# Performance work log

Measured on AMD Instinct MI355X. Metric: run time of the kernel, lower is better.

The kernel has to match this reference:

```python
import jax, jax.numpy as jnp
import numpy as np

B, C, N = 64, 512, 512  # batch, channels (=in_dim), last dim (=in_dim)
OUT = 512
GROUPS = 32
EPS = 1e-5


def setup_inputs() -> dict:
    key = jax.random.key(0)
    ks = jax.random.split(key, 7)
    s = 1.0 / np.sqrt(C)
    return {
        "x": jax.random.normal(ks[0], (B, C, N), dtype=jnp.float32),
        "q_w": jax.random.normal(ks[1], (OUT, C), dtype=jnp.float32) * s,
        "q_b": jax.random.normal(ks[2], (OUT,), dtype=jnp.float32) * s,
        "k_w": jax.random.normal(ks[3], (OUT, C), dtype=jnp.float32) * s,
        "k_b": jax.random.normal(ks[4], (OUT,), dtype=jnp.float32) * s,
        "v_w": jax.random.normal(ks[5], (OUT, C), dtype=jnp.float32) * s,
        "v_b": jax.random.normal(ks[6], (OUT,), dtype=jnp.float32) * s,
        "gn_w": jnp.ones((C,), dtype=jnp.float32),
        "gn_b": jnp.zeros((C,), dtype=jnp.float32),
    }


def group_norm(x, w, b):
    # x: (B, C, N); 32 groups over channel dim, affine per-channel.
    Bb, Cc, Nn = x.shape
    xg = x.reshape(Bb, GROUPS, -1)
    mean = jnp.mean(xg, axis=-1, keepdims=True)
    var = jnp.var(xg, axis=-1, keepdims=True)
    xn = ((xg - mean) * jax.lax.rsqrt(var + EPS)).reshape(Bb, Cc, Nn)
    return xn * w[None, :, None] + b[None, :, None]


def reference(x, q_w, q_b, k_w, k_b, v_w, v_b, gn_w, gn_b):
    xn = group_norm(x, gn_w, gn_b)  # (B, C, N)
    # nn.Linear applies to the last dim (N == in_dim)
    q = jnp.einsum("bcn,dn->bcd", xn, q_w) + q_b  # (B, C, OUT)
    k = jnp.einsum("bcn,dn->bcd", xn, k_w) + k_b
    v = jnp.einsum("bcn,dn->bcd", xn, v_w) + v_b
    scale = 1.0 / jnp.sqrt(jnp.float32(OUT))
    scores = jnp.einsum("bqd,bkd->bqk", q, k) * scale  # (B, C, C)
    attn = jax.nn.softmax(scores, axis=-1)
    return jnp.einsum("bqk,bkd->bqd", attn, v)  # (B, C, OUT)
```

## Files before the change

### kernel.cpp

```cpp
#include <hip/hip_runtime.h>
#include <cstdint>

#define EPSV 1e-5f
#define SM_SCALE 0.044194173824159216f

typedef unsigned short u16;
typedef __attribute__((ext_vector_type(8))) short short8;
typedef __attribute__((ext_vector_type(4))) float f32x4;

__device__ __forceinline__ u16 f2bf(float f) {
  union { float f; uint32_t u; } v; v.f = f;
  return (u16)((v.u + 0x7FFFu + ((v.u >> 16) & 1u)) >> 16);
}

__device__ __forceinline__ void gload_lds16(const void* g, void* l) {
  __builtin_amdgcn_global_load_lds((const __attribute__((address_space(1))) void*)g,
                                   (__attribute__((address_space(3))) void*)l, 16, 0, 0);
}

__device__ __forceinline__ f32x4 mfma16(short8 a, short8 b, f32x4 c) {
  return __builtin_amdgcn_mfma_f32_16x16x32_bf16(a, b, c, 0, 0, 0);
}

__device__ __forceinline__ const short8* lds_frag(const u16* t, int row, int cc) {
  return reinterpret_cast<const short8*>(t + (size_t)(((row << 2) + (cc ^ ((row >> 1) & 3))) << 3));
}

#define WAIT_ENTER(N, is_tail)                                      \
  if (is_tail) { asm volatile("s_waitcnt vmcnt(0)" ::: "memory"); } \
  else         { asm volatile("s_waitcnt vmcnt(" #N ")" ::: "memory"); } \
  __builtin_amdgcn_s_barrier();                                     \
  asm volatile("" ::: "memory");

#define WAIT_EXIT()                                                 \
  asm volatile("s_waitcnt lgkmcnt(0)" ::: "memory");                \
  __builtin_amdgcn_s_barrier();                                     \
  asm volatile("" ::: "memory");

__global__ __launch_bounds__(256) void gn_fused_k(const float* __restrict__ x,
                                                  const float* __restrict__ gw,
                                                  const float* __restrict__ gb,
                                                  u16* __restrict__ xn) {
  __shared__ float xs[8192];
  __shared__ float ls[4], lss[4];
  const int bg = blockIdx.x;
  const int g = bg & 31;
  const float* p = x + (size_t)bg * 8192;
  float s = 0.f, ss = 0.f;
#pragma unroll
  for (int i = 0; i < 8; ++i) {
    const int idx = i * 1024 + threadIdx.x * 4;
    float4 v = *reinterpret_cast<const float4*>(p + idx);
    *reinterpret_cast<float4*>(xs + idx) = v;
    s += v.x + v.y + v.z + v.w;
    ss += v.x * v.x + v.y * v.y + v.z * v.z + v.w * v.w;
  }
  for (int off = 32; off; off >>= 1) { s += __shfl_xor(s, off); ss += __shfl_xor(ss, off); }
  const int w = threadIdx.x >> 6;
  if ((threadIdx.x & 63) == 0) { ls[w] = s; lss[w] = ss; }
  __syncthreads();
  s = ls[0] + ls[1] + ls[2] + ls[3];
  ss = lss[0] + lss[1] + lss[2] + lss[3];
  const float inv_n = 1.0f / 8192.f;
  const float mean = s * inv_n;
  const float rstd = rsqrtf(ss * inv_n - mean * mean + EPSV);
#pragma unroll
  for (int j = 0; j < 4; ++j) {
    const int idx = j * 2048 + threadIdx.x * 8;
    const int c = g * 16 + (idx >> 9);
    const float sc = gw[c] * rstd;
    const float sh = gb[c] - mean * sc;
    u16 o[8];
#pragma unroll
    for (int e = 0; e < 8; ++e) o[e] = f2bf(xs[idx + e] * sc + sh);
    *reinterpret_cast<uint4*>(xn + (size_t)bg * 8192 + idx) = *reinterpret_cast<const uint4*>(o);
  }
}

__global__ __launch_bounds__(256) void cast3_k(const float* __restrict__ a,
                                               const float* __restrict__ b2,
                                               const float* __restrict__ c,
                                               u16* __restrict__ oa, u16* __restrict__ ob,
                                               u16* __restrict__ oc) {
  const int which = blockIdx.x >> 7;
  const float* in = which == 0 ? a : (which == 1 ? b2 : c);
  u16* out = which == 0 ? oa : (which == 1 ? ob : oc);
  size_t base = (((size_t)(blockIdx.x & 127)) * 256 + threadIdx.x) * 8;
  float4 v0 = *reinterpret_cast<const float4*>(in + base);
  float4 v1 = *reinterpret_cast<const float4*>(in + base + 4);
  u16 o[8];
  o[0] = f2bf(v0.x); o[1] = f2bf(v0.y); o[2] = f2bf(v0.z); o[3] = f2bf(v0.w);
  o[4] = f2bf(v1.x); o[5] = f2bf(v1.y); o[6] = f2bf(v1.z); o[7] = f2bf(v1.w);
  *reinterpret_cast<uint4*>(out + base) = *reinterpret_cast<const uint4*>(o);
}

template <int OUT_MODE>
__global__ __launch_bounds__(512, 1) void gemm256_k(const u16* __restrict__ A, size_t sA,
                                                    const u16* __restrict__ Bm, size_t sB,
                                                    const float* __restrict__ bias,
                                                    void* __restrict__ out, size_t sO) {
  __shared__ u16 smem[65536];
  const int d = blockIdx.x;
  const int wgid = (d & 7) * 32 + (d >> 3);
  const int b = wgid >> 2;
  const int tile = wgid & 3;
  const int tm = (tile >> 1) * 256, tn = (tile & 1) * 256;
  const u16* Ab = A + (size_t)b * sA;
  const u16* Bb = Bm + (size_t)b * sB;
  const int tid = threadIdx.x, w = tid >> 6, lane = tid & 63;
  const int rh = w >> 2, cw = w & 3;
  const int frow = lane & 15, cc = lane >> 4;
  f32x4 acc[8][4] = {};
  short8 af[8], bfr[2];

#define STAGEH(Lofs, Gp)                                                       \
  {                                                                            \
    const u16* gsrc_ = (Gp);                                                   \
    _Pragma("unroll")                                                          \
    for (int p_ = 0; p_ < 2; ++p_) {                                           \
      const int row_ = p_ * 64 + (tid >> 3);                                   \
      const int slot_ = (tid & 7) ^ (row_ & 7);                                \
      gload_lds16(gsrc_ + (size_t)row_ * 512 + slot_ * 8,                      \
                  &smem[(Lofs) + p_ * 4096 + tid * 8]);                        \
    }                                                                          \
  }

#define PHASE(VMN, QB, KS, CP, ...)                                            \
  {                                                                            \
    asm volatile("s_waitcnt vmcnt(" #VMN ")" ::: "memory");                    \
    __builtin_amdgcn_s_barrier();                                              \
    asm volatile("" ::: "memory");                                             \
    _Pragma("unroll")                                                          \
    for (int j_ = 0; j_ < 2; ++j_) {                                           \
      const int lrb_ = (cw & 1) * 64 + (CP) * 32 + j_ * 16 + frow;             \
      bfr[j_] = *reinterpret_cast<const short8*>(                              \
          &smem[(QB) + 16384 + (cw >> 1) * 8192 + lrb_ * 64 +                  \
                (((KS) * 4 + cc) ^ (lrb_ & 7)) * 8]);                          \
    }                                                                          \
    if ((CP) == 0) {                                                           \
      _Pragma("unroll")                                                        \
      for (int ri_ = 0; ri_ < 8; ++ri_) {                                      \
        const int lra_ = ri_ * 16 + frow;                                      \
        af[ri_] = *reinterpret_cast<const short8*>(                            \
            &smem[(QB) + rh * 8192 + lra_ * 64 +                               \
                  (((KS) * 4 + cc) ^ (lra_ & 7)) * 8]);                        \
      }                                                                        \
    }                                                                          \
    __VA_ARGS__                                                                \
    __builtin_amdgcn_s_setprio(1);                                             \
    _Pragma("unroll")                                                          \
    for (int ri_ = 0; ri_ < 8; ++ri_) {                                        \
      acc[ri_][(CP) * 2]     = mfma16(af[ri_], bfr[0], acc[ri_][(CP) * 2]);    \
      acc[ri_][(CP) * 2 + 1] = mfma16(af[ri_], bfr[1], acc[ri_][(CP) * 2 + 1]);\
    }                                                                          \
    __builtin_amdgcn_s_setprio(0);                                             \
    __builtin_amdgcn_s_barrier();                                              \
    asm volatile("" ::: "memory");                                             \
  }

  STAGEH(0,     Ab + (size_t)tm * 512);
  STAGEH(8192,  Ab + (size_t)(tm + 128) * 512);
  STAGEH(16384, Bb + (size_t)tn * 512);
  STAGEH(24576, Bb + (size_t)(tn + 128) * 512);
  STAGEH(32768, Ab + (size_t)tm * 512 + 64);

  for (int i = 0; i < 3; ++i) {
    const int k0c1 = i * 128 + 64;
    const int k0n2 = i * 128 + 128;
    const int k0n3 = i * 128 + 192;
    PHASE(2, 0, 0, 0,
          STAGEH(40960, Ab + (size_t)(tm + 128) * 512 + k0c1);
          STAGEH(49152, Bb + (size_t)tn * 512 + k0c1);)
    PHASE(6, 0, 0, 1,
          STAGEH(57344, Bb + (size_t)(tn + 128) * 512 + k0c1);)
    PHASE(6, 0, 1, 0, )
    PHASE(2, 0, 1, 1,
          STAGEH(0, Ab + (size_t)tm * 512 + k0n2);)
    PHASE(2, 32768, 0, 0,
          STAGEH(8192,  Ab + (size_t)(tm + 128) * 512 + k0n2);
          STAGEH(16384, Bb + (size_t)tn * 512 + k0n2);)
    PHASE(6, 32768, 0, 1,
          STAGEH(24576, Bb + (size_t)(tn + 128) * 512 + k0n2);)
    PHASE(6, 32768, 1, 0, )
    PHASE(2, 32768, 1, 1,
          STAGEH(32768, Ab + (size_t)tm * 512 + k0n3);)
  }
  PHASE(2, 0, 0, 0,
        STAGEH(40960, Ab + (size_t)(tm + 128) * 512 + 448);
        STAGEH(49152, Bb + (size_t)tn * 512 + 448);)
  PHASE(6, 0, 0, 1,
        STAGEH(57344, Bb + (size_t)(tn + 128) * 512 + 448);)
  PHASE(6, 0, 1, 0, )
  PHASE(2, 0, 1, 1, )
  PHASE(0, 32768, 0, 0, )
  PHASE(0, 32768, 0, 1, )
  PHASE(0, 32768, 1, 0, )
  PHASE(0, 32768, 1, 1, )
#undef PHASE
#undef STAGEH

  const int col0 = lane & 15, row0 = (lane >> 4) * 4;
#pragma unroll
  for (int ri = 0; ri < 8; ++ri) {
#pragma unroll
    for (int cj = 0; cj < 4; ++cj) {
      const int gc = tn + cw * 64 + cj * 16 + col0;
      const float bv = (OUT_MODE == 0) ? bias[gc] : 0.f;
#pragma unroll
      for (int r = 0; r < 4; ++r) {
        const int gr = tm + rh * 128 + ri * 16 + row0 + r;
        float v = acc[ri][cj][r];
        if (OUT_MODE == 0) v += bv;
        if (OUT_MODE == 1) v += bias[gr];
        if (OUT_MODE == 2)
          ((float*)out)[(size_t)b * sO + (size_t)gr * 512 + gc] = v;
        else
          ((u16*)out)[(size_t)b * sO + (size_t)gr * 512 + gc] = f2bf(v);
      }
    }
  }
}

__global__ __launch_bounds__(256, 2) void scores_softmax_k(const u16* __restrict__ Q,
                                                           const u16* __restrict__ K,
                                                           u16* __restrict__ P) {
  __shared__ u16 Qs[2][2048];
  __shared__ u16 Ks[2][16384];
  __shared__ float rmax[4][64], rsum[4][64];
  const int d = blockIdx.x;
  const int t = d >> 3;
  const int b = (d & 7) * 8 + (t >> 3);
  const int m0 = (t & 7) * 64;
  const u16* Qb = Q + (size_t)b * 262144 + (size_t)m0 * 512;
  const u16* Kb = K + (size_t)b * 262144;
  u16* Pb = P + (size_t)b * 262144;
  const int tid = threadIdx.x, kq = tid >> 6, lane = tid & 63;
  const int srow = lane >> 2;
  const int ssw = ((lane & 3) ^ ((lane >> 3) & 3)) * 8;
  f32x4 acc[4][8] = {};

#define SC_STAGE(bb, k0)                                                       \
  {                                                                            \
    _Pragma("unroll")                                                          \
    for (int s2 = 0; s2 < 8; ++s2) {                                           \
      const int c = kq * 8 + s2;                                               \
      gload_lds16(Kb + (size_t)(c * 16 + srow) * 512 + (k0) + ssw,             \
                  &Ks[bb][c * 512]);                                           \
    }                                                                          \
    gload_lds16(Qb + (size_t)(kq * 16 + srow) * 512 + (k0) + ssw,              \
                &Qs[bb][kq * 512]);                                            \
  }

  SC_STAGE(0, 0);
  SC_STAGE(1, 32);
  for (int ts = 0; ts < 16; ++ts) {
    const int cur = ts & 1;
    WAIT_ENTER(9, ts == 15);
    const int frow = lane & 15, cc = lane >> 4;
    short8 aq[4];
#pragma unroll
    for (int i = 0; i < 4; ++i)
      aq[i] = *lds_frag(Qs[cur], i * 16 + frow, cc);
#pragma unroll
    for (int j = 0; j < 8; ++j) {
      short8 bk = *lds_frag(Ks[cur], kq * 128 + j * 16 + frow, cc);
#pragma unroll
      for (int i = 0; i < 4; ++i)
        acc[i][j] = mfma16(aq[i], bk, acc[i][j]);
    }
    WAIT_EXIT();
    if (ts < 14) SC_STAGE(cur, (ts + 2) * 32);
  }
#undef SC_STAGE

  float pm[4][4];
#pragma unroll
  for (int i = 0; i < 4; ++i)
#pragma unroll
    for (int r = 0; r < 4; ++r) pm[i][r] = -1e30f;
#pragma unroll
  for (int i = 0; i < 4; ++i)
#pragma unroll
    for (int j = 0; j < 8; ++j)
#pragma unroll
      for (int r = 0; r < 4; ++r) {
        float v = acc[i][j][r] * SM_SCALE;
        acc[i][j][r] = v;
        pm[i][r] = fmaxf(pm[i][r], v);
      }
#pragma unroll
  for (int off = 1; off < 16; off <<= 1)
#pragma unroll
    for (int i = 0; i < 4; ++i)
#pragma unroll
      for (int r = 0; r < 4; ++r) pm[i][r] = fmaxf(pm[i][r], __shfl_xor(pm[i][r], off));
  if ((lane & 15) == 0) {
#pragma unroll
    for (int i = 0; i < 4; ++i)
#pragma unroll
      for (int r = 0; r < 4; ++r)
        rmax[kq][i * 16 + (lane >> 4) * 4 + r] = pm[i][r];
  }
  __syncthreads();
#pragma unroll
  for (int i = 0; i < 4; ++i)
#pragma unroll
    for (int r = 0; r < 4; ++r) {
      const int row = i * 16 + (lane >> 4) * 4 + r;
      pm[i][r] = fmaxf(fmaxf(rmax[0][row], rmax[1][row]), fmaxf(rmax[2][row], rmax[3][row]));
    }
  float ps[4][4];
#pragma unroll
  for (int i = 0; i < 4; ++i)
#pragma unroll
    for (int r = 0; r < 4; ++r) ps[i][r] = 0.f;
#pragma unroll
  for (int i = 0; i < 4; ++i)
#pragma unroll
    for (int j = 0; j < 8; ++j)
#pragma unroll
      for (int r = 0; r < 4; ++r) {
        float e = __expf(acc[i][j][r] - pm[i][r]);
        acc[i][j][r] = e;
        ps[i][r] += e;
      }
#pragma unroll
  for (int off = 1; off < 16; off <<= 1)
#pragma unroll
    for (int i = 0; i < 4; ++i)
#pragma unroll
      for (int r = 0; r < 4; ++r) ps[i][r] += __shfl_xor(ps[i][r], off);
  if ((lane & 15) == 0) {
#pragma unroll
    for (int i = 0; i < 4; ++i)
#pragma unroll
      for (int r = 0; r < 4; ++r)
        rsum[kq][i * 16 + (lane >> 4) * 4 + r] = ps[i][r];
  }
  __syncthreads();
#pragma unroll
  for (int i = 0; i < 4; ++i)
#pragma unroll
    for (int r = 0; r < 4; ++r) {
      const int row = i * 16 + (lane >> 4) * 4 + r;
      ps[i][r] = 1.0f / (rsum[0][row] + rsum[1][row] + rsum[2][row] + rsum[3][row]);
    }
#pragma unroll
  for (int i = 0; i < 4; ++i)
#pragma unroll
    for (int j = 0; j < 8; ++j) {
      const int gcol = kq * 128 + j * 16 + (lane & 15);
#pragma unroll
      for (int r = 0; r < 4; ++r) {
        const int grow = m0 + i * 16 + (lane >> 4) * 4 + r;
        Pb[(size_t)grow * 512 + gcol] = f2bf(acc[i][j][r] * ps[i][r]);
      }
    }
}

extern "C" void kernel_launch(void* const* d_in, const int* in_sizes, int n_in,
                              void* d_out, int out_size, void* d_ws, size_t ws_size,
                              hipStream_t stream) {
  const float* x = (const float*)d_in[0];
  const float* qw = (const float*)d_in[1];
  const float* qb = (const float*)d_in[2];
  const float* kw = (const float*)d_in[3];
  const float* kb = (const float*)d_in[4];
  const float* vw = (const float*)d_in[5];
  const float* vb = (const float*)d_in[6];
  const float* gnw = (const float*)d_in[7];
  const float* gnb = (const float*)d_in[8];

  char* ws = (char*)d_ws;
  u16* qwb = (u16*)(ws);
  u16* kwb = (u16*)(ws + 524288);
  u16* vwb = (u16*)(ws + 2 * 524288);
  u16* xn = (u16*)(ws + 4 * 524288);
  u16* Qb = xn + 16777216;
  u16* Kb = Qb + 16777216;
  u16* VT = Kb + 16777216;
  u16* P = xn;
  float* out = (float*)d_out;

  gn_fused_k<<<dim3(2048), dim3(256), 0, stream>>>(x, gnw, gnb, xn);
  cast3_k<<<dim3(384), dim3(256), 0, stream>>>(qw, kw, vw, qwb, kwb, vwb);
  gemm256_k<0><<<dim3(256), dim3(512), 0, stream>>>(xn, (size_t)262144, qwb, (size_t)0, qb, (void*)Qb, (size_t)262144);
  gemm256_k<0><<<dim3(256), dim3(512), 0, stream>>>(xn, (size_t)262144, kwb, (size_t)0, kb, (void*)Kb, (size_t)262144);
  gemm256_k<1><<<dim3(256), dim3(512), 0, stream>>>(vwb, (size_t)0, xn, (size_t)262144, vb, (void*)VT, (size_t)262144);
  scores_softmax_k<<<dim3(512), dim3(256), 0, stream>>>(Qb, Kb, P);
  gemm256_k<2><<<dim3(256), dim3(512), 0, stream>>>(P, (size_t)262144, VT, (size_t)262144, (const float*)nullptr, (void*)out, (size_t)262144);
}
```

Before: 148.1 us.

## Retile scores-softmax kernel to 128-row blocks with 8 waves and triple buffering

Rewrites the fused QK^T plus softmax kernel so each 512-thread workgroup handles 128 query rows instead of 64, with 8 waves each owning 64 key columns. This halves how often each K tile is reloaded per batch. The K/Q staging moves to a three-slot ring, with the next load issued after fragments are read so that only one barrier is needed per k-step. MFMA sections run at raised wave priority. The costs are a larger accumulator (32 fragments per wave), more LDS, one workgroup per CU and 256 blocks, which reduces occupancy and latency hiding.

```diff
diff --git a/kernel.cpp b/kernel.cpp
--- a/kernel.cpp
+++ b/kernel.cpp
@@ -21,21 +21,6 @@
 __device__ __forceinline__ f32x4 mfma16(short8 a, short8 b, f32x4 c) {
   return __builtin_amdgcn_mfma_f32_16x16x32_bf16(a, b, c, 0, 0, 0);
 }
-
-__device__ __forceinline__ const short8* lds_frag(const u16* t, int row, int cc) {
-  return reinterpret_cast<const short8*>(t + (size_t)(((row << 2) + (cc ^ ((row >> 1) & 3))) << 3));
-}
-
-#define WAIT_ENTER(N, is_tail)                                      \
-  if (is_tail) { asm volatile("s_waitcnt vmcnt(0)" ::: "memory"); } \
-  else         { asm volatile("s_waitcnt vmcnt(" #N ")" ::: "memory"); } \
-  __builtin_amdgcn_s_barrier();                                     \
-  asm volatile("" ::: "memory");
-
-#define WAIT_EXIT()                                                 \
-  asm volatile("s_waitcnt lgkmcnt(0)" ::: "memory");                \
-  __builtin_amdgcn_s_barrier();                                     \
-  asm volatile("" ::: "memory");
 
 __global__ __launch_bounds__(256) void gn_fused_k(const float* __restrict__ x,
                                                   const float* __restrict__ gw,
@@ -221,139 +206,156 @@
   }
 }
 
-__global__ __launch_bounds__(256, 2) void scores_softmax_k(const u16* __restrict__ Q,
+__global__ __launch_bounds__(512, 1) void scores_softmax_k(const u16* __restrict__ Q,
                                                            const u16* __restrict__ K,
                                                            u16* __restrict__ P) {
-  __shared__ u16 Qs[2][2048];
-  __shared__ u16 Ks[2][16384];
-  __shared__ float rmax[4][64], rsum[4][64];
+  __shared__ u16 smem[61440];
+  __shared__ float rmax[128][8], rsum[128][8];
   const int d = blockIdx.x;
-  const int t = d >> 3;
-  const int b = (d & 7) * 8 + (t >> 3);
-  const int m0 = (t & 7) * 64;
+  const int wgid = (d & 7) * 32 + (d >> 3);
+  const int b = wgid >> 2;
+  const int m0 = (wgid & 3) * 128;
   const u16* Qb = Q + (size_t)b * 262144 + (size_t)m0 * 512;
   const u16* Kb = K + (size_t)b * 262144;
-  u16* Pb = P + (size_t)b * 262144;
-  const int tid = threadIdx.x, kq = tid >> 6, lane = tid & 63;
-  const int srow = lane >> 2;
-  const int ssw = ((lane & 3) ^ ((lane >> 3) & 3)) * 8;
-  f32x4 acc[4][8] = {};
-
-#define SC_STAGE(bb, k0)                                                       \
+  u16* Pb = P + (size_t)b * 262144 + (size_t)m0 * 512;
+  const int tid = threadIdx.x, w = tid >> 6, lane = tid & 63;
+  const int frow = lane & 15, cc = lane >> 4;
+  f32x4 acc[8][4] = {};
+
+#define KQ_STAGE(m, k0)                                                        \
   {                                                                            \
     _Pragma("unroll")                                                          \
-    for (int s2 = 0; s2 < 8; ++s2) {                                           \
-      const int c = kq * 8 + s2;                                               \
-      gload_lds16(Kb + (size_t)(c * 16 + srow) * 512 + (k0) + ssw,             \
-                  &Ks[bb][c * 512]);                                           \
-    }                                                                          \
-    gload_lds16(Qb + (size_t)(kq * 16 + srow) * 512 + (k0) + ssw,              \
-                &Qs[bb][kq * 512]);                                            \
-  }
-
-  SC_STAGE(0, 0);
-  SC_STAGE(1, 32);
+    for (int s2_ = 0; s2_ < 4; ++s2_) {                                        \
+      const int idx_ = s2_ * 512 + tid;                                        \
+      const int row_ = idx_ >> 2, slot_ = idx_ & 3;                            \
+      gload_lds16(Kb + (size_t)row_ * 512 + (k0) + (slot_ ^ ((row_ >> 1) & 3)) * 8, \
+                  &smem[(m) * 16384 + idx_ * 8]);                              \
+    }                                                                          \
+    {                                                                          \
+      const int row_ = tid >> 2, slot_ = tid & 3;                              \
+      gload_lds16(Qb + (size_t)row_ * 512 + (k0) + (slot_ ^ ((row_ >> 1) & 3)) * 8, \
+                  &smem[49152 + (m) * 4096 + tid * 8]);                        \
+    }                                                                          \
+  }
+
+  KQ_STAGE(0, 0);
+  KQ_STAGE(1, 32);
   for (int ts = 0; ts < 16; ++ts) {
-    const int cur = ts & 1;
-    WAIT_ENTER(9, ts == 15);
-    const int frow = lane & 15, cc = lane >> 4;
-    short8 aq[4];
-#pragma unroll
-    for (int i = 0; i < 4; ++i)
-      aq[i] = *lds_frag(Qs[cur], i * 16 + frow, cc);
-#pragma unroll
-    for (int j = 0; j < 8; ++j) {
-      short8 bk = *lds_frag(Ks[cur], kq * 128 + j * 16 + frow, cc);
-#pragma unroll
-      for (int i = 0; i < 4; ++i)
-        acc[i][j] = mfma16(aq[i], bk, acc[i][j]);
-    }
-    WAIT_EXIT();
-    if (ts < 14) SC_STAGE(cur, (ts + 2) * 32);
-  }
-#undef SC_STAGE
-
-  float pm[4][4];
-#pragma unroll
-  for (int i = 0; i < 4; ++i)
-#pragma unroll
-    for (int r = 0; r < 4; ++r) pm[i][r] = -1e30f;
-#pragma unroll
-  for (int i = 0; i < 4; ++i)
-#pragma unroll
-    for (int j = 0; j < 8; ++j)
+    const int m = ts % 3;
+    if (ts < 15) { asm volatile("s_waitcnt vmcnt(5)" ::: "memory"); }
+    else         { asm volatile("s_waitcnt vmcnt(0)" ::: "memory"); }
+    __builtin_amdgcn_s_barrier();
+    asm volatile("" ::: "memory");
+    const u16* Kbuf = &smem[m * 16384];
+    const u16* Qbuf = &smem[49152 + m * 4096];
+    short8 af[8], bf[4];
+#pragma unroll
+    for (int ri = 0; ri < 8; ++ri) {
+      const int qrow = ri * 16 + frow;
+      af[ri] = *reinterpret_cast<const short8*>(
+          &Qbuf[qrow * 32 + ((cc ^ ((qrow >> 1) & 3)) * 8)]);
+    }
+#pragma unroll
+    for (int cj = 0; cj < 4; ++cj) {
+      const int krow = w * 64 + cj * 16 + frow;
+      bf[cj] = *reinterpret_cast<const short8*>(
+          &Kbuf[krow * 32 + ((cc ^ ((krow >> 1) & 3)) * 8)]);
+    }
+    if (ts < 14) KQ_STAGE((ts + 2) % 3, (ts + 2) * 32);
+    __builtin_amdgcn_s_setprio(1);
+#pragma unroll
+    for (int ri = 0; ri < 8; ++ri)
+#pragma unroll
+      for (int cj = 0; cj < 4; ++cj)
+        acc[ri][cj] = mfma16(af[ri], bf[cj], acc[ri][cj]);
+    __builtin_amdgcn_s_setprio(0);
+  }
+#undef KQ_STAGE
+
+  float pm[8][4];
+#pragma unroll
+  for (int ri = 0; ri < 8; ++ri)
+#pragma unroll
+    for (int r = 0; r < 4; ++r) pm[ri][r] = -1e30f;
+#pragma unroll
+  for (int ri = 0; ri < 8; ++ri)
+#pragma unroll
+    for (int cj = 0; cj < 4; ++cj)
 #pragma unroll
       for (int r = 0; r < 4; ++r) {
-        float v = acc[i][j][r] * SM_SCALE;
-        acc[i][j][r] = v;
-        pm[i][r] = fmaxf(pm[i][r], v);
+        float v = acc[ri][cj][r] * SM_SCALE;
+        acc[ri][cj][r] = v;
+        pm[ri][r] = fmaxf(pm[ri][r], v);
       }
 #pragma unroll
   for (int off = 1; off < 16; off <<= 1)
 #pragma unroll
-    for (int i = 0; i < 4; ++i)
-#pragma unroll
-      for (int r = 0; r < 4; ++r) pm[i][r] = fmaxf(pm[i][r], __shfl_xor(pm[i][r], off));
-  if ((lane & 15) == 0) {
-#pragma unroll
-    for (int i = 0; i < 4; ++i)
-#pragma unroll
-      for (int r = 0; r < 4; ++r)
-        rmax[kq][i * 16 + (lane >> 4) * 4 + r] = pm[i][r];
+    for (int ri = 0; ri < 8; ++ri)
+#pragma unroll
+      for (int r = 0; r < 4; ++r) pm[ri][r] = fmaxf(pm[ri][r], __shfl_xor(pm[ri][r], off));
+  if (frow == 0) {
+#pragma unroll
+    for (int ri = 0; ri < 8; ++ri)
+#pragma unroll
+      for (int r = 0; r < 4; ++r) rmax[ri * 16 + cc * 4 + r][w] = pm[ri][r];
   }
   __syncthreads();
 #pragma unroll
-  for (int i = 0; i < 4; ++i)
+  for (int ri = 0; ri < 8; ++ri)
 #pragma unroll
     for (int r = 0; r < 4; ++r) {
-      const int row = i * 16 + (lane >> 4) * 4 + r;
-      pm[i][r] = fmaxf(fmaxf(rmax[0][row], rmax[1][row]), fmaxf(rmax[2][row], rmax[3][row]));
-    }
-  float ps[4][4];
-#pragma unroll
-  for (int i = 0; i < 4; ++i)
-#pragma unroll
-    for (int r = 0; r < 4; ++r) ps[i][r] = 0.f;
-#pragma unroll
-  for (int i = 0; i < 4; ++i)
-#pragma unroll
-    for (int j = 0; j < 8; ++j)
+      const int row = ri * 16 + cc * 4 + r;
+      float4 a = *reinterpret_cast<const float4*>(&rmax[row][0]);
+      float4 b4 = *reinterpret_cast<const float4*>(&rmax[row][4]);
+      pm[ri][r] = fmaxf(fmaxf(fmaxf(a.x, a.y), fmaxf(a.z, a.w)),
+                        fmaxf(fmaxf(b4.x, b4.y), fmaxf(b4.z, b4.w)));
+    }
+  float ps[8][4];
+#pragma unroll
+  for (int ri = 0; ri < 8; ++ri)
+#pragma unroll
+    for (int r = 0; r < 4; ++r) ps[ri][r] = 0.f;
+#pragma unroll
+  for (int ri = 0; ri < 8; ++ri)
+#pragma unroll
+    for (int cj = 0; cj < 4; ++cj)
 #pragma unroll
       for (int r = 0; r < 4; ++r) {
-        float e = __expf(acc[i][j][r] - pm[i][r]);
-        acc[i][j][r] = e;
-        ps[i][r] += e;
+        float e = __expf(acc[ri][cj][r] - pm[ri][r]);
+        acc[ri][cj][r] = e;
+        ps[ri][r] += e;
       }
 #pragma unroll
   for (int off = 1; off < 16; off <<= 1)
 #pragma unroll
-    for (int i = 0; i < 4; ++i)
-#pragma unroll
-      for (int r = 0; r < 4; ++r) ps[i][r] += __shfl_xor(ps[i][r], off);
-  if ((lane & 15) == 0) {
-#pragma unroll
-    for (int i = 0; i < 4; ++i)
-#pragma unroll
-      for (int r = 0; r < 4; ++r)
-        rsum[kq][i * 16 + (lane >> 4) * 4 + r] = ps[i][r];
+    for (int ri = 0; ri < 8; ++ri)
+#pragma unroll
+      for (int r = 0; r < 4; ++r) ps[ri][r] += __shfl_xor(ps[ri][r], off);
+  if (frow == 0) {
+#pragma unroll
+    for (int ri = 0; ri < 8; ++ri)
+#pragma unroll
+      for (int r = 0; r < 4; ++r) rsum[ri * 16 + cc * 4 + r][w] = ps[ri][r];
   }
   __syncthreads();
 #pragma unroll
-  for (int i = 0; i < 4; ++i)
+  for (int ri = 0; ri < 8; ++ri)
 #pragma unroll
     for (int r = 0; r < 4; ++r) {
-      const int row = i * 16 + (lane >> 4) * 4 + r;
-      ps[i][r] = 1.0f / (rsum[0][row] + rsum[1][row] + rsum[2][row] + rsum[3][row]);
-    }
-#pragma unroll
-  for (int i = 0; i < 4; ++i)
-#pragma unroll
-    for (int j = 0; j < 8; ++j) {
-      const int gcol = kq * 128 + j * 16 + (lane & 15);
+      const int row = ri * 16 + cc * 4 + r;
+      float4 a = *reinterpret_cast<const float4*>(&rsum[row][0]);
+      float4 b4 = *reinterpret_cast<const float4*>(&rsum[row][4]);
+      ps[ri][r] = 1.0f / (a.x + a.y + a.z + a.w + b4.x + b4.y + b4.z + b4.w);
+    }
+#pragma unroll
+  for (int ri = 0; ri < 8; ++ri)
+#pragma unroll
+    for (int cj = 0; cj < 4; ++cj) {
+      const int gcol = w * 64 + cj * 16 + frow;
 #pragma unroll
       for (int r = 0; r < 4; ++r) {
-        const int grow = m0 + i * 16 + (lane >> 4) * 4 + r;
-        Pb[(size_t)grow * 512 + gcol] = f2bf(acc[i][j][r] * ps[i][r]);
+        const int grow = ri * 16 + cc * 4 + r;
+        Pb[(size_t)grow * 512 + gcol] = f2bf(acc[ri][cj][r] * ps[ri][r]);
       }
     }
 }
@@ -387,6 +389,6 @@
   gemm256_k<0><<<dim3(256), dim3(512), 0, stream>>>(xn, (size_t)262144, qwb, (size_t)0, qb, (void*)Qb, (size_t)262144);
   gemm256_k<0><<<dim3(256), dim3(512), 0, stream>>>(xn, (size_t)262144, kwb, (size_t)0, kb, (void*)Kb, (size_t)262144);
   gemm256_k<1><<<dim3(256), dim3(512), 0, stream>>>(vwb, (size_t)0, xn, (size_t)262144, vb, (void*)VT, (size_t)262144);
-  scores_softmax_k<<<dim3(512), dim3(256), 0, stream>>>(Qb, Kb, P);
+  scores_softmax_k<<<dim3(256), dim3(512), 0, stream>>>(Qb, Kb, P);
   gemm256_k<2><<<dim3(256), dim3(512), 0, stream>>>(P, (size_t)262144, VT, (size_t)262144, (const float*)nullptr, (void*)out, (size_t)262144);
 }
```

After: 148.3 us. No clear change (+0.2%).

## Split fused scores-softmax into tiled GEMM plus standalone row-softmax kernel

Applied to the files above, without the earlier changes.

Replaces the fused QK^T plus softmax kernel with two steps. The existing 256-tile GEMM, in a bias-free bf16-output mode, writes the raw scores, and a new lightweight kernel applies scale, max, exp and normalisation per row in place. The aim is to reuse the better-tuned GEMM tiling for the score product instead of the 64-row fused kernel. The cost is an extra read and write of the full bf16 score matrix. Scores are also rounded to bf16 before the softmax, which lowers accuracy.

```diff
diff --git a/kernel.cpp b/kernel.cpp
--- a/kernel.cpp
+++ b/kernel.cpp
@@ -13,6 +13,10 @@
   return (u16)((v.u + 0x7FFFu + ((v.u >> 16) & 1u)) >> 16);
 }
 
+__device__ __forceinline__ float bf2f(u16 h) {
+  union { uint32_t u; float f; } v; v.u = ((uint32_t)h) << 16; return v.f;
+}
+
 __device__ __forceinline__ void gload_lds16(const void* g, void* l) {
   __builtin_amdgcn_global_load_lds((const __attribute__((address_space(1))) void*)g,
                                    (__attribute__((address_space(3))) void*)l, 16, 0, 0);
@@ -21,21 +25,6 @@
 __device__ __forceinline__ f32x4 mfma16(short8 a, short8 b, f32x4 c) {
   return __builtin_amdgcn_mfma_f32_16x16x32_bf16(a, b, c, 0, 0, 0);
 }
-
-__device__ __forceinline__ const short8* lds_frag(const u16* t, int row, int cc) {
-  return reinterpret_cast<const short8*>(t + (size_t)(((row << 2) + (cc ^ ((row >> 1) & 3))) << 3));
-}
-
-#define WAIT_ENTER(N, is_tail)                                      \
-  if (is_tail) { asm volatile("s_waitcnt vmcnt(0)" ::: "memory"); } \
-  else         { asm volatile("s_waitcnt vmcnt(" #N ")" ::: "memory"); } \
-  __builtin_amdgcn_s_barrier();                                     \
-  asm volatile("" ::: "memory");
-
-#define WAIT_EXIT()                                                 \
-  asm volatile("s_waitcnt lgkmcnt(0)" ::: "memory");                \
-  __builtin_amdgcn_s_barrier();                                     \
-  asm volatile("" ::: "memory");
 
 __global__ __launch_bounds__(256) void gn_fused_k(const float* __restrict__ x,
                                                   const float* __restrict__ gw,
@@ -221,141 +210,30 @@
   }
 }
 
-__global__ __launch_bounds__(256, 2) void scores_softmax_k(const u16* __restrict__ Q,
-                                                           const u16* __restrict__ K,
-                                                           u16* __restrict__ P) {
-  __shared__ u16 Qs[2][2048];
-  __shared__ u16 Ks[2][16384];
-  __shared__ float rmax[4][64], rsum[4][64];
-  const int d = blockIdx.x;
-  const int t = d >> 3;
-  const int b = (d & 7) * 8 + (t >> 3);
-  const int m0 = (t & 7) * 64;
-  const u16* Qb = Q + (size_t)b * 262144 + (size_t)m0 * 512;
-  const u16* Kb = K + (size_t)b * 262144;
-  u16* Pb = P + (size_t)b * 262144;
-  const int tid = threadIdx.x, kq = tid >> 6, lane = tid & 63;
-  const int srow = lane >> 2;
-  const int ssw = ((lane & 3) ^ ((lane >> 3) & 3)) * 8;
-  f32x4 acc[4][8] = {};
-
-#define SC_STAGE(bb, k0)                                                       \
-  {                                                                            \
-    _Pragma("unroll")                                                          \
-    for (int s2 = 0; s2 < 8; ++s2) {                                           \
-      const int c = kq * 8 + s2;                                               \
-      gload_lds16(Kb + (size_t)(c * 16 + srow) * 512 + (k0) + ssw,             \
-                  &Ks[bb][c * 512]);                                           \
-    }                                                                          \
-    gload_lds16(Qb + (size_t)(kq * 16 + srow) * 512 + (k0) + ssw,              \
-                &Qs[bb][kq * 512]);                                            \
-  }
-
-  SC_STAGE(0, 0);
-  SC_STAGE(1, 32);
-  for (int ts = 0; ts < 16; ++ts) {
-    const int cur = ts & 1;
-    WAIT_ENTER(9, ts == 15);
-    const int frow = lane & 15, cc = lane >> 4;
-    short8 aq[4];
-#pragma unroll
-    for (int i = 0; i < 4; ++i)
-      aq[i] = *lds_frag(Qs[cur], i * 16 + frow, cc);
-#pragma unroll
-    for (int j = 0; j < 8; ++j) {
-      short8 bk = *lds_frag(Ks[cur], kq * 128 + j * 16 + frow, cc);
-#pragma unroll
-      for (int i = 0; i < 4; ++i)
-        acc[i][j] = mfma16(aq[i], bk, acc[i][j]);
-    }
-    WAIT_EXIT();
-    if (ts < 14) SC_STAGE(cur, (ts + 2) * 32);
-  }
-#undef SC_STAGE
-
-  float pm[4][4];
-#pragma unroll
-  for (int i = 0; i < 4; ++i)
-#pragma unroll
-    for (int r = 0; r < 4; ++r) pm[i][r] = -1e30f;
-#pragma unroll
-  for (int i = 0; i < 4; ++i)
-#pragma unroll
-    for (int j = 0; j < 8; ++j)
-#pragma unroll
-      for (int r = 0; r < 4; ++r) {
-        float v = acc[i][j][r] * SM_SCALE;
-        acc[i][j][r] = v;
-        pm[i][r] = fmaxf(pm[i][r], v);
-      }
-#pragma unroll
-  for (int off = 1; off < 16; off <<= 1)
-#pragma unroll
-    for (int i = 0; i < 4; ++i)
-#pragma unroll
-      for (int r = 0; r < 4; ++r) pm[i][r] = fmaxf(pm[i][r], __shfl_xor(pm[i][r], off));
-  if ((lane & 15) == 0) {
-#pragma unroll
-    for (int i = 0; i < 4; ++i)
-#pragma unroll
-      for (int r = 0; r < 4; ++r)
-        rmax[kq][i * 16 + (lane >> 4) * 4 + r] = pm[i][r];
-  }
-  __syncthreads();
-#pragma unroll
-  for (int i = 0; i < 4; ++i)
-#pragma unroll
-    for (int r = 0; r < 4; ++r) {
-      const int row = i * 16 + (lane >> 4) * 4 + r;
-      pm[i][r] = fmaxf(fmaxf(rmax[0][row], rmax[1][row]), fmaxf(rmax[2][row], rmax[3][row]));
-    }
-  float ps[4][4];
-#pragma unroll
-  for (int i = 0; i < 4; ++i)
-#pragma unroll
-    for (int r = 0; r < 4; ++r) ps[i][r] = 0.f;
-#pragma unroll
-  for (int i = 0; i < 4; ++i)
-#pragma unroll
-    for (int j = 0; j < 8; ++j)
-#pragma unroll
-      for (int r = 0; r < 4; ++r) {
-        float e = __expf(acc[i][j][r] - pm[i][r]);
-        acc[i][j][r] = e;
-        ps[i][r] += e;
-      }
-#pragma unroll
-  for (int off = 1; off < 16; off <<= 1)
-#pragma unroll
-    for (int i = 0; i < 4; ++i)
-#pragma unroll
-      for (int r = 0; r < 4; ++r) ps[i][r] += __shfl_xor(ps[i][r], off);
-  if ((lane & 15) == 0) {
-#pragma unroll
-    for (int i = 0; i < 4; ++i)
-#pragma unroll
-      for (int r = 0; r < 4; ++r)
-        rsum[kq][i * 16 + (lane >> 4) * 4 + r] = ps[i][r];
-  }
-  __syncthreads();
-#pragma unroll
-  for (int i = 0; i < 4; ++i)
-#pragma unroll
-    for (int r = 0; r < 4; ++r) {
-      const int row = i * 16 + (lane >> 4) * 4 + r;
-      ps[i][r] = 1.0f / (rsum[0][row] + rsum[1][row] + rsum[2][row] + rsum[3][row]);
-    }
-#pragma unroll
-  for (int i = 0; i < 4; ++i)
-#pragma unroll
-    for (int j = 0; j < 8; ++j) {
-      const int gcol = kq * 128 + j * 16 + (lane & 15);
-#pragma unroll
-      for (int r = 0; r < 4; ++r) {
-        const int grow = m0 + i * 16 + (lane >> 4) * 4 + r;
-        Pb[(size_t)grow * 512 + gcol] = f2bf(acc[i][j][r] * ps[i][r]);
-      }
-    }
+__global__ __launch_bounds__(256) void rowsm_k(u16* __restrict__ S) {
+  const int w = threadIdx.x >> 6, lane = threadIdx.x & 63;
+  const size_t rbase = (size_t)blockIdx.x * 64 + (size_t)w * 16;
+#pragma unroll 4
+  for (int r = 0; r < 16; ++r) {
+    u16* row = S + (rbase + r) * 512 + lane * 8;
+    short8 v = *reinterpret_cast<const short8*>(row);
+    float f[8];
+#pragma unroll
+    for (int e = 0; e < 8; ++e) f[e] = bf2f((u16)v[e]) * SM_SCALE;
+    float m = f[0];
+#pragma unroll
+    for (int e = 1; e < 8; ++e) m = fmaxf(m, f[e]);
+    for (int off = 32; off; off >>= 1) m = fmaxf(m, __shfl_xor(m, off));
+    float s = 0.f;
+#pragma unroll
+    for (int e = 0; e < 8; ++e) { f[e] = __expf(f[e] - m); s += f[e]; }
+    for (int off = 32; off; off >>= 1) s += __shfl_xor(s, off);
+    const float inv = 1.0f / s;
+    u16 o[8];
+#pragma unroll
+    for (int e = 0; e < 8; ++e) o[e] = f2bf(f[e] * inv);
+    *reinterpret_cast<uint4*>(row) = *reinterpret_cast<const uint4*>(o);
+  }
 }
 
 extern "C" void kernel_launch(void* const* d_in, const int* in_sizes, int n_in,
@@ -379,7 +257,7 @@
   u16* Qb = xn + 16777216;
   u16* Kb = Qb + 16777216;
   u16* VT = Kb + 16777216;
-  u16* P = xn;
+  u16* S = xn;
   float* out = (float*)d_out;
 
   gn_fused_k<<<dim3(2048), dim3(256), 0, stream>>>(x, gnw, gnb, xn);
@@ -387,6 +265,7 @@
   gemm256_k<0><<<dim3(256), dim3(512), 0, stream>>>(xn, (size_t)262144, qwb, (size_t)0, qb, (void*)Qb, (size_t)262144);
   gemm256_k<0><<<dim3(256), dim3(512), 0, stream>>>(xn, (size_t)262144, kwb, (size_t)0, kb, (void*)Kb, (size_t)262144);
   gemm256_k<1><<<dim3(256), dim3(512), 0, stream>>>(vwb, (size_t)0, xn, (size_t)262144, vb, (void*)VT, (size_t)262144);
-  scores_softmax_k<<<dim3(512), dim3(256), 0, stream>>>(Qb, Kb, P);
-  gemm256_k<2><<<dim3(256), dim3(512), 0, stream>>>(P, (size_t)262144, VT, (size_t)262144, (const float*)nullptr, (void*)out, (size_t)262144);
-}
+  gemm256_k<3><<<dim3(256), dim3(512), 0, stream>>>(Qb, (size_t)262144, Kb, (size_t)262144, (const float*)nullptr, (void*)S, (size_t)262144);
+  rowsm_k<<<dim3(512), dim3(256), 0, stream>>>(S);
+  gemm256_k<2><<<dim3(256), dim3(512), 0, stream>>>(S, (size_t)262144, VT, (size_t)262144, (const float*)nullptr, (void*)out, (size_t)262144);
+}
```

Result: no change. 149.8 us (+1.2%).
